# Kernel tuning notes

Hardware: AMD Instinct MI355X
Metric: run time of the kernel (lower is better)

The kernel has to match this reference:

```python
import jax, jax.numpy as jnp
import numpy as np

NE, NR, D, B = 1_000_000, 1000, 32, 1_048_576
CURV = 1.0  # curvature K
HALF = D // 2


def _project(spatial):
    # recompute time component so point lies on hyperboloid <x,x>_L = -1/K
    x0 = jnp.sqrt(1.0 / CURV + jnp.sum(spatial * spatial, axis=-1, keepdims=True))
    return jnp.concatenate([x0, spatial], axis=-1)


def _lorentz_inner(u, v):
    return -u[..., 0] * v[..., 0] + jnp.sum(u[..., 1:] * v[..., 1:], axis=-1)


def setup_inputs() -> dict:
    key = jax.random.key(0)
    k0, k1, k2, k3, k4, k5, k6, k7 = jax.random.split(key, 8)
    tangent = jax.random.normal(k0, (NE, D), dtype=jnp.float32) * 0.01
    x0 = jnp.sqrt(1.0 / CURV + jnp.sum(tangent * tangent, axis=-1, keepdims=True))
    entity_emb = jnp.concatenate([x0, tangent], axis=-1)  # [NE, D+1]
    rel_boost_w = jax.random.normal(k1, (NR, D), dtype=jnp.float32) * 0.01
    rel_rot_w = jax.random.normal(k2, (NR, D), dtype=jnp.float32) * 0.01  # torch init is zeros; small noise for a nontrivial test
    rel_trans_w = jax.random.normal(k3, (NR, D), dtype=jnp.float32) * 0.01
    ent_bias_w = jax.random.normal(k4, (NE, 1), dtype=jnp.float32) * 0.01
    heads = jax.random.randint(k5, (B,), 0, NE)
    relations = jax.random.randint(k6, (B,), 0, NR)
    tails = jax.random.randint(k7, (B,), 0, NE)
    return {"heads": heads, "relations": relations, "tails": tails,
            "entity_emb": entity_emb, "rel_boost_w": rel_boost_w,
            "rel_rot_w": rel_rot_w, "rel_trans_w": rel_trans_w,
            "ent_bias_w": ent_bias_w}


def reference(heads, relations, tails, entity_emb, rel_boost_w, rel_rot_w, rel_trans_w, ent_bias_w):
    h = entity_emb[heads]                      # [B, D+1]
    t = entity_emb[tails]                      # [B, D+1]
    boost = rel_boost_w[relations]             # [B, D]
    rotation = rel_rot_w[relations]            # [B, D]
    translation = rel_trans_w[relations]       # [B, D]

    # --- spatial rotation: pairwise Givens rotations (i, i+HALF) ---
    x0 = h[..., 0:1]
    sp = h[..., 1:]
    a, b = sp[..., :HALF], sp[..., HALF:]
    c = jnp.cos(rotation[..., :HALF])
    s = jnp.sin(rotation[..., :HALF])
    rotated = jnp.concatenate([c * a - s * b, s * a + c * b], axis=-1)
    h_rot = jnp.concatenate([x0, rotated], axis=-1)

    # --- Lorentz boost along first spatial axis (only rapidity[..., 0] used) ---
    rap = jnp.clip(boost, -2.0, 2.0)
    c0 = jnp.cosh(rap[..., 0:1])
    s0 = jnp.sinh(rap[..., 0:1])
    bx0 = h_rot[..., 0:1]
    bx1 = h_rot[..., 1:2]
    new_x1 = bx0 * s0 + bx1 * c0
    new_spatial = jnp.concatenate([new_x1, h_rot[..., 2:]], axis=-1)
    h_boost = _project(new_spatial)  # time component recomputed by projection

    # --- exp map with tangent v = 0.1 * [0, translation] ---
    v = jnp.concatenate([jnp.zeros_like(translation[..., 0:1]), translation], axis=-1) * 0.1
    vn = jnp.sqrt(jnp.clip(_lorentz_inner(v, v), 1e-6, None))[..., None]
    res = jnp.cosh(vn) * h_boost + jnp.sinh(vn) * v / vn
    h_trans = _project(res[..., 1:])

    # --- Lorentz distance and score ---
    inner = _lorentz_inner(h_trans, t)
    ic = jnp.clip(-inner * CURV, 1.0 + 1e-6, None)
    dist = (1.0 / np.sqrt(CURV)) * jnp.arccosh(ic)
    b_h = ent_bias_w[heads][..., 0]
    b_t = ent_bias_w[tails][..., 0]
    return -dist * dist + b_h + b_t
```

## Files before the change

### kernel.cpp

```cpp
#include <hip/hip_runtime.h>
#include <math.h>

#define NR_ 1000
#define D_ 32
#define HALF_ 16
#define EMB_DIM 33
#define TAB_STRIDE 68
#define ROWF (64 * EMB_DIM)

__global__ __launch_bounds__(256) void rel_precompute_kernel(
    const float* __restrict__ boost_w, const float* __restrict__ rot_w,
    const float* __restrict__ trans_w, float* __restrict__ tab) {
  int r = blockIdx.x * blockDim.x + threadIdx.x;
  if (r >= NR_) return;
  const float* ro = rot_w   + (size_t)r * D_;
  const float* tr = trans_w + (size_t)r * D_;
  float* o = tab + (size_t)r * TAB_STRIDE;
  #pragma unroll
  for (int j = 0; j < HALF_; ++j) {
    float th = ro[j];
    o[j]         = cosf(th);
    o[HALF_ + j] = sinf(th);
  }
  float s2 = 0.f;
  #pragma unroll
  for (int j = 0; j < D_; ++j) { float v = tr[j]; s2 = fmaf(v, v, s2); }
  float vn  = sqrtf(fmaxf(0.01f * s2, 1e-6f));
  float k   = sinhf(vn) / vn * 0.1f;
  #pragma unroll
  for (int j = 0; j < D_; ++j) o[2 * HALF_ + j] = k * tr[j];
  float rap = fminf(fmaxf(boost_w[(size_t)r * D_], -2.f), 2.f);
  o[64] = coshf(rap);
  o[65] = sinhf(rap);
  o[66] = coshf(vn);
  o[67] = 0.f;
}

__global__ __launch_bounds__(256) void lorentz_coop_kernel(
    const int* __restrict__ heads, const int* __restrict__ rels,
    const int* __restrict__ tails, const float* __restrict__ emb,
    const float* __restrict__ bias, const float* __restrict__ tab,
    float* __restrict__ out, int n) {
  __shared__ float lds_row[4][ROWF];
  __shared__ int   lds_hidx[4][64];
  __shared__ int   lds_tidx[4][64];

  const int lane = threadIdx.x & 63;
  const int w    = threadIdx.x >> 6;
  const int gid  = blockIdx.x * 256 + threadIdx.x;
  const int i    = (gid < n) ? gid : (n - 1);

  const int hd = heads[i];
  const int rl = rels[i];
  const int tl = tails[i];
  lds_hidx[w][lane] = hd;
  lds_tidx[w][lane] = tl;

  const float b_h = bias[hd];
  const float b_t = bias[tl];
  const float4* __restrict__ T =
      reinterpret_cast<const float4*>(tab + (size_t)rl * TAB_STRIDE);

  float* __restrict__ rowbuf = lds_row[w];
  __syncthreads();

  #pragma unroll
  for (int k = 0; k < EMB_DIM; ++k) {
    int idx = k * 64 + lane;
    int e   = (idx * 993) >> 15;
    int j   = idx - e * 33;
    int row = lds_hidx[w][e];
    rowbuf[idx] = emb[(size_t)((long long)row * EMB_DIM + j)];
  }
  __syncthreads();

  const float* __restrict__ my = rowbuf + lane * EMB_DIM;
  float x0 = my[0];
  float r[D_];
  #pragma unroll
  for (int q = 0; q < 4; ++q) {
    float4 cv = T[q];
    float4 sv = T[4 + q];
    float cj[4] = {cv.x, cv.y, cv.z, cv.w};
    float sj[4] = {sv.x, sv.y, sv.z, sv.w};
    #pragma unroll
    for (int m = 0; m < 4; ++m) {
      int j = 4 * q + m;
      float a = my[1 + j];
      float b = my[1 + HALF_ + j];
      r[j]         = cj[m] * a - sj[m] * b;
      r[HALF_ + j] = sj[m] * a + cj[m] * b;
    }
  }
  float4 hv = T[16];
  r[0] = fmaf(x0, hv.y, r[0] * hv.x);
  const float cvn = hv.z;

  float rs[D_];
  float n2 = 0.f;
  #pragma unroll
  for (int q = 0; q < 8; ++q) {
    float4 kv = T[8 + q];
    float kj[4] = {kv.x, kv.y, kv.z, kv.w};
    #pragma unroll
    for (int m = 0; m < 4; ++m) {
      int j = 4 * q + m;
      rs[j] = fmaf(cvn, r[j], kj[m]);
      n2 = fmaf(rs[j], rs[j], n2);
    }
  }
  const float ht0 = sqrtf(1.f + n2);

  __syncthreads();

  #pragma unroll
  for (int k = 0; k < EMB_DIM; ++k) {
    int idx = k * 64 + lane;
    int e   = (idx * 993) >> 15;
    int j   = idx - e * 33;
    int row = lds_tidx[w][e];
    rowbuf[idx] = emb[(size_t)((long long)row * EMB_DIM + j)];
  }
  __syncthreads();

  const float t0 = my[0];
  float dot = 0.f;
  #pragma unroll
  for (int j = 0; j < D_; ++j) dot = fmaf(rs[j], my[1 + j], dot);

  float neg_inner = fmaf(ht0, t0, -dot);
  float ic   = fmaxf(neg_inner, 1.0f + 1e-6f);
  float dist = acoshf(ic);
  if (gid < n) out[gid] = b_h + b_t - dist * dist;
}

__global__ __launch_bounds__(256) void lorentz_fallback_kernel(
    const int* __restrict__ heads, const int* __restrict__ rels,
    const int* __restrict__ tails, const float* __restrict__ emb,
    const float* __restrict__ boost_w, const float* __restrict__ rot_w,
    const float* __restrict__ trans_w, const float* __restrict__ bias,
    float* __restrict__ out, int n) {
  int i = blockIdx.x * blockDim.x + threadIdx.x;
  if (i >= n) return;
  int hd = heads[i], rl = rels[i], tl = tails[i];
  const float* hrow = emb + (size_t)hd * EMB_DIM;
  const float* trow = emb + (size_t)tl * EMB_DIM;
  const float* ro = rot_w   + (size_t)rl * D_;
  const float* tr = trans_w + (size_t)rl * D_;
  float c[HALF_], s[HALF_], kt[D_];
  #pragma unroll
  for (int j = 0; j < HALF_; ++j) { float th = ro[j]; c[j] = cosf(th); s[j] = sinf(th); }
  float s2 = 0.f;
  #pragma unroll
  for (int j = 0; j < D_; ++j) { float v = tr[j]; s2 = fmaf(v, v, s2); }
  float vn = sqrtf(fmaxf(0.01f * s2, 1e-6f));
  float cvn = coshf(vn);
  float k = sinhf(vn) / vn * 0.1f;
  #pragma unroll
  for (int j = 0; j < D_; ++j) kt[j] = k * tr[j];
  float rap = fminf(fmaxf(boost_w[(size_t)rl * D_], -2.f), 2.f);
  float c0 = coshf(rap), s0 = sinhf(rap);
  float x0 = hrow[0];
  float r[D_];
  #pragma unroll
  for (int j = 0; j < HALF_; ++j) {
    float a = hrow[1 + j], b = hrow[1 + HALF_ + j];
    r[j] = c[j] * a - s[j] * b;
    r[HALF_ + j] = s[j] * a + c[j] * b;
  }
  r[0] = fmaf(x0, s0, r[0] * c0);
  float t0 = trow[0], n2 = 0.f, dot = 0.f;
  #pragma unroll
  for (int j = 0; j < D_; ++j) {
    float rsv = fmaf(cvn, r[j], kt[j]);
    n2  = fmaf(rsv, rsv, n2);
    dot = fmaf(rsv, trow[1 + j], dot);
  }
  float ht0 = sqrtf(1.f + n2);
  float neg_inner = fmaf(ht0, t0, -dot);
  float ic = fmaxf(neg_inner, 1.0f + 1e-6f);
  float dist = acoshf(ic);
  out[i] = bias[hd] + bias[tl] - dist * dist;
}

extern "C" void kernel_launch(void* const* d_in, const int* in_sizes, int n_in,
                              void* d_out, int out_size, void* d_ws, size_t ws_size,
                              hipStream_t stream) {
  const int*   heads  = (const int*)d_in[0];
  const int*   rels   = (const int*)d_in[1];
  const int*   tails  = (const int*)d_in[2];
  const float* emb    = (const float*)d_in[3];
  const float* boostw = (const float*)d_in[4];
  const float* rotw   = (const float*)d_in[5];
  const float* transw = (const float*)d_in[6];
  const float* bias   = (const float*)d_in[7];
  float* out = (float*)d_out;
  int n = in_sizes[0];

  size_t tab_bytes = (size_t)NR_ * TAB_STRIDE * sizeof(float);
  dim3 block(256);
  dim3 grid((n + 255) / 256);

  if (ws_size >= tab_bytes) {
    float* tab = (float*)d_ws;
    rel_precompute_kernel<<<dim3((NR_ + 255) / 256), block, 0, stream>>>(
        boostw, rotw, transw, tab);
    lorentz_coop_kernel<<<grid, block, 0, stream>>>(
        heads, rels, tails, emb, bias, tab, out, n);
  } else {
    lorentz_fallback_kernel<<<grid, block, 0, stream>>>(
        heads, rels, tails, emb, boostw, rotw, transw, bias, out, n);
  }
}
```

Measured before the change: 295.3 us.

## Gather embedding rows via wave readlane into swizzled per-wave LDS, drop block barriers

Replaces the LDS index tables and block-wide __syncthreads with wave-local cooperative gathers. Each wave uses readlane to broadcast row indices so half-waves load one 32-float spatial row each, coalesced. Rows land in a rotated (swizzled) LDS layout to avoid bank conflicts, and tail rows are prefetched into registers before the head computation, overlapping their latency. The time component is loaded separately per thread, launch bounds ask for 5 blocks per CU, and register pressure rises with two 32-float staging arrays. No barrier separates LDS writes from cross-lane reads; this relies on wave-synchronous execution within a single wave.

```diff
diff --git a/kernel.cpp b/kernel.cpp
--- a/kernel.cpp
+++ b/kernel.cpp
@@ -6,7 +6,6 @@
 #define HALF_ 16
 #define EMB_DIM 33
 #define TAB_STRIDE 68
-#define ROWF (64 * EMB_DIM)
 
 __global__ __launch_bounds__(256) void rel_precompute_kernel(
     const float* __restrict__ boost_w, const float* __restrict__ rot_w,
@@ -36,14 +35,12 @@
   o[67] = 0.f;
 }
 
-__global__ __launch_bounds__(256) void lorentz_coop_kernel(
+__global__ __launch_bounds__(256, 5) void lorentz_ws_kernel(
     const int* __restrict__ heads, const int* __restrict__ rels,
     const int* __restrict__ tails, const float* __restrict__ emb,
     const float* __restrict__ bias, const float* __restrict__ tab,
     float* __restrict__ out, int n) {
-  __shared__ float lds_row[4][ROWF];
-  __shared__ int   lds_hidx[4][64];
-  __shared__ int   lds_tidx[4][64];
+  __shared__ float buf[4][2048];
 
   const int lane = threadIdx.x & 63;
   const int w    = threadIdx.x >> 6;
@@ -53,29 +50,40 @@
   const int hd = heads[i];
   const int rl = rels[i];
   const int tl = tails[i];
-  lds_hidx[w][lane] = hd;
-  lds_tidx[w][lane] = tl;
-
-  const float b_h = bias[hd];
-  const float b_t = bias[tl];
+
+  const float x0   = emb[(size_t)hd * EMB_DIM];
+  const float t0   = emb[(size_t)tl * EMB_DIM];
+  const float bsum = bias[hd] + bias[tl];
   const float4* __restrict__ T =
       reinterpret_cast<const float4*>(tab + (size_t)rl * TAB_STRIDE);
 
-  float* __restrict__ rowbuf = lds_row[w];
-  __syncthreads();
-
-  #pragma unroll
-  for (int k = 0; k < EMB_DIM; ++k) {
-    int idx = k * 64 + lane;
-    int e   = (idx * 993) >> 15;
-    int j   = idx - e * 33;
-    int row = lds_hidx[w][e];
-    rowbuf[idx] = emb[(size_t)((long long)row * EMB_DIM + j)];
-  }
-  __syncthreads();
-
-  const float* __restrict__ my = rowbuf + lane * EMB_DIM;
-  float x0 = my[0];
+  float* __restrict__ rb = buf[w];
+  const int half = lane >> 5;
+  const int jj   = lane & 31;
+
+  float hv[32];
+  #pragma unroll
+  for (int k = 0; k < 32; ++k) {
+    int r0  = __builtin_amdgcn_readlane(hd, 2 * k);
+    int r1  = __builtin_amdgcn_readlane(hd, 2 * k + 1);
+    int row = half ? r1 : r0;
+    hv[k] = emb[(size_t)row * EMB_DIM + 1 + jj];
+  }
+  #pragma unroll
+  for (int k = 0; k < 32; ++k) {
+    int e = 2 * k + half;
+    rb[(e << 5) | ((jj + e) & 31)] = hv[k];
+  }
+
+  float tv[32];
+  #pragma unroll
+  for (int k = 0; k < 32; ++k) {
+    int r0  = __builtin_amdgcn_readlane(tl, 2 * k);
+    int r1  = __builtin_amdgcn_readlane(tl, 2 * k + 1);
+    int row = half ? r1 : r0;
+    tv[k] = emb[(size_t)row * EMB_DIM + 1 + jj];
+  }
+
   float r[D_];
   #pragma unroll
   for (int q = 0; q < 4; ++q) {
@@ -86,15 +94,15 @@
     #pragma unroll
     for (int m = 0; m < 4; ++m) {
       int j = 4 * q + m;
-      float a = my[1 + j];
-      float b = my[1 + HALF_ + j];
+      float a = rb[(lane << 5) | ((j + lane) & 31)];
+      float b = rb[(lane << 5) | ((j + 16 + lane) & 31)];
       r[j]         = cj[m] * a - sj[m] * b;
       r[HALF_ + j] = sj[m] * a + cj[m] * b;
     }
   }
-  float4 hv = T[16];
-  r[0] = fmaf(x0, hv.y, r[0] * hv.x);
-  const float cvn = hv.z;
+  float4 hv4 = T[16];
+  r[0] = fmaf(x0, hv4.y, r[0] * hv4.x);
+  const float cvn = hv4.z;
 
   float rs[D_];
   float n2 = 0.f;
@@ -111,27 +119,22 @@
   }
   const float ht0 = sqrtf(1.f + n2);
 
-  __syncthreads();
-
-  #pragma unroll
-  for (int k = 0; k < EMB_DIM; ++k) {
-    int idx = k * 64 + lane;
-    int e   = (idx * 993) >> 15;
-    int j   = idx - e * 33;
-    int row = lds_tidx[w][e];
-    rowbuf[idx] = emb[(size_t)((long long)row * EMB_DIM + j)];
-  }
-  __syncthreads();
-
-  const float t0 = my[0];
+  #pragma unroll
+  for (int k = 0; k < 32; ++k) {
+    int e = 2 * k + half;
+    rb[(e << 5) | ((jj + e) & 31)] = tv[k];
+  }
   float dot = 0.f;
   #pragma unroll
-  for (int j = 0; j < D_; ++j) dot = fmaf(rs[j], my[1 + j], dot);
+  for (int j = 0; j < D_; ++j) {
+    float tj = rb[(lane << 5) | ((j + lane) & 31)];
+    dot = fmaf(rs[j], tj, dot);
+  }
 
   float neg_inner = fmaf(ht0, t0, -dot);
   float ic   = fmaxf(neg_inner, 1.0f + 1e-6f);
   float dist = acoshf(ic);
-  if (gid < n) out[gid] = b_h + b_t - dist * dist;
+  if (gid < n) out[gid] = bsum - dist * dist;
 }
 
 __global__ __launch_bounds__(256) void lorentz_fallback_kernel(
@@ -205,7 +208,7 @@
     float* tab = (float*)d_ws;
     rel_precompute_kernel<<<dim3((NR_ + 255) / 256), block, 0, stream>>>(
         boostw, rotw, transw, tab);
-    lorentz_coop_kernel<<<grid, block, 0, stream>>>(
+    lorentz_ws_kernel<<<grid, block, 0, stream>>>(
         heads, rels, tails, emb, bias, tab, out, n);
   } else {
     lorentz_fallback_kernel<<<grid, block, 0, stream>>>(
```

Measured after the change: 382.5 us. 1.3x slower.
